# Performance work log

Hardware: AMD Instinct MI355X
Metric: run time of the kernel (lower is better)

## Reference

```python
import jax, jax.numpy as jnp
import numpy as np

G = 56          # voxel grid resolution per axis
N = 65536
K = 27          # 3x3x3 kernel offsets
C_IN = 128
C_OUT = 128


def _build_rulebook():
    """Submanifold conv rulebook: for each kernel offset, (input_row, output_row) pairs.

    Padded to P=N pairs per offset; invalid pairs use in_idx=0 and out_idx=N
    (a dummy output slot that is dropped), so shapes are static.
    """
    rng = np.random.default_rng(0)
    keys = np.sort(rng.choice(G ** 3, size=N, replace=False)).astype(np.int64)
    x = keys // (G * G)
    y = (keys // G) % G
    z = keys % G
    in_idx = np.zeros((K, N), dtype=np.int32)
    out_idx = np.full((K, N), N, dtype=np.int32)
    k = 0
    for dx in (-1, 0, 1):
        for dy in (-1, 0, 1):
            for dz in (-1, 0, 1):
                nx, ny, nz = x + dx, y + dy, z + dz
                valid = (nx >= 0) & (nx < G) & (ny >= 0) & (ny < G) & (nz >= 0) & (nz < G)
                nkey = (nx * G + ny) * G + nz
                pos = np.searchsorted(keys, np.clip(nkey, 0, G ** 3 - 1))
                pos = np.clip(pos, 0, N - 1)
                found = valid & (keys[pos] == nkey)
                cnt = int(found.sum())
                in_idx[k, :cnt] = pos[found]
                out_idx[k, :cnt] = np.nonzero(found)[0]
                k += 1
    return jnp.asarray(in_idx), jnp.asarray(out_idx)


def setup_inputs() -> dict:
    key = jax.random.key(0)
    k1, k2, k3 = jax.random.split(key, 3)
    fan_in = K * C_IN
    features = jax.random.normal(k1, (N, C_IN), dtype=jnp.float32)
    weight = jax.random.normal(k2, (K, C_IN, C_OUT), dtype=jnp.float32) * (1.0 / np.sqrt(fan_in))
    bias = jax.random.normal(k3, (C_OUT,), dtype=jnp.float32) * 0.01
    in_idx, out_idx = _build_rulebook()
    return {"features": features, "weight": weight, "bias": bias,
            "in_idx": in_idx, "out_idx": out_idx}


def reference(features, weight, bias, in_idx, out_idx):
    # gather: [K, P, C_in]
    gathered = features[in_idx]
    # per-offset GEMM: [K, P, C_out]
    contrib = jnp.einsum('kpc,kcd->kpd', gathered, weight)
    n = features.shape[0]
    c_out = weight.shape[-1]
    # scatter-accumulate into N real rows + 1 dummy row for padded pairs
    out = jnp.zeros((n + 1, c_out), dtype=features.dtype)
    out = out.at[out_idx.reshape(-1)].add(contrib.reshape(-1, c_out))
    return out[:n] + bias
```

## Files before the change

### kernel.cpp

```cpp
#include <hip/hip_runtime.h>
#include <hip/hip_bf16.h>
#include <stdint.h>

#define NV   65536
#define KOFF 27
#define CIN  128
#define COUT 128

typedef __bf16 bf16x8 __attribute__((ext_vector_type(8)));
typedef float  f32x4  __attribute__((ext_vector_type(4)));

__device__ __forceinline__ void async_copy16(void* lds, const void* g) {
    __builtin_amdgcn_global_load_lds(
        (const __attribute__((address_space(1))) void*)g,
        (__attribute__((address_space(3))) void*)lds,
        16, 0, 0);
}


__global__ void k_prep_feat(const float* __restrict__ f,
                            __hip_bfloat16* __restrict__ fb,
                            int total, int nvalid) {
    int i = blockIdx.x * 256 + threadIdx.x;
    if (i < total) {
        float v = (i < nvalid) ? f[i] : 0.0f;
        fb[i] = __float2bfloat16(v);
    }
}

__global__ void k_prep_w(const float* __restrict__ w,
                         __hip_bfloat16* __restrict__ wt) {
    int i = blockIdx.x * 256 + threadIdx.x;
    if (i < KOFF * CIN * COUT) {
        int k    = i >> 14;
        int cin  = (i >> 7) & 127;
        int cout = i & 127;
        wt[k * 16384 + cout * 128 + cin] = __float2bfloat16(w[i]);
    }
}

__global__ void k_init_nbr(int* __restrict__ nbr, int total) {
    int i = blockIdx.x * 256 + threadIdx.x;
    if (i < total) nbr[i] = NV;
}

__global__ void k_scatter_nbr(const int* __restrict__ in_idx,
                              const int* __restrict__ out_idx,
                              int* __restrict__ nbr) {
    int i = blockIdx.x * 256 + threadIdx.x;
    if (i < KOFF * NV) {
        int k = i >> 16;
        int o = out_idx[i];
        nbr[k * (NV + 1) + o] = in_idx[i];
    }
}

__global__ __launch_bounds__(256, 2)
void sp_conv_main(const __hip_bfloat16* __restrict__ feats,
                  const __hip_bfloat16* __restrict__ wt,
                  const int* __restrict__ nbr,
                  const float* __restrict__ bias,
                  float* __restrict__ out) {
    __shared__ unsigned char smem[65536];
    unsigned char* smA = smem;
    unsigned char* smB = smem + 32768;

    const int t   = threadIdx.x;
    const int bid = blockIdx.x;
    const int tile0 = ((bid & 7) * 64 + (bid >> 3)) * 128;

    const int w    = t >> 6;
    const int lane = t & 63;
    const int lr   = lane & 15;
    const int quad = lane >> 4;
    const int m0   = (w >> 1) * 64;
    const int n0   = (w & 1) * 64;

    const int srow   = t >> 4;
    const int sbyte  = ((t & 15) ^ srow) * 16;

    f32x4 acc[4][4] = {};

    const unsigned char* featsB = (const unsigned char*)feats;
    const unsigned char* wtB    = (const unsigned char*)wt;

    for (int k = 0; k < KOFF; ++k) {
        const int* nbrk = nbr + k * (NV + 1) + tile0;
        const unsigned char* wk = wtB + (size_t)k * 32768;
        #pragma unroll
        for (int i = 0; i < 8; ++i) {
            int r = i * 16 + srow;
            int arow = nbrk[r];
            async_copy16(smA + i * 4096 + t * 16,
                         featsB + (size_t)arow * 256 + sbyte);
            async_copy16(smB + i * 4096 + t * 16,
                         wk + r * 256 + sbyte);
        }
        __syncthreads();

        #pragma unroll
        for (int ks = 0; ks < 4; ++ks) {
            bf16x8 af[4], bfr[4];
            #pragma unroll
            for (int mt = 0; mt < 4; ++mt) {
                int row = m0 + mt * 16 + lr;
                int pch = ((ks * 4 + quad) ^ lr) * 16;
                af[mt] = *(const bf16x8*)(smA + row * 256 + pch);
            }
            #pragma unroll
            for (int nt = 0; nt < 4; ++nt) {
                int row = n0 + nt * 16 + lr;
                int pch = ((ks * 4 + quad) ^ lr) * 16;
                bfr[nt] = *(const bf16x8*)(smB + row * 256 + pch);
            }
            #pragma unroll
            for (int mt = 0; mt < 4; ++mt)
                #pragma unroll
                for (int nt = 0; nt < 4; ++nt)
                    acc[mt][nt] = __builtin_amdgcn_mfma_f32_16x16x32_bf16(
                        af[mt], bfr[nt], acc[mt][nt], 0, 0, 0);
        }
        __syncthreads();
    }

    float bv[4];
    #pragma unroll
    for (int nt = 0; nt < 4; ++nt) bv[nt] = bias[n0 + nt * 16 + lr];

    #pragma unroll
    for (int mt = 0; mt < 4; ++mt) {
        #pragma unroll
        for (int nt = 0; nt < 4; ++nt) {
            #pragma unroll
            for (int r = 0; r < 4; ++r) {
                int grow = tile0 + m0 + mt * 16 + quad * 4 + r;
                out[(size_t)grow * COUT + n0 + nt * 16 + lr] =
                    acc[mt][nt][r] + bv[nt];
            }
        }
    }
}


extern "C" void kernel_launch(void* const* d_in, const int* in_sizes, int n_in,
                              void* d_out, int out_size, void* d_ws, size_t ws_size,
                              hipStream_t stream) {
    const float* features = (const float*)d_in[0];
    const float* weight   = (const float*)d_in[1];
    const float* bias     = (const float*)d_in[2];
    const int*   in_idx   = (const int*)d_in[3];
    const int*   out_idx  = (const int*)d_in[4];
    float* out = (float*)d_out;

    uint8_t* ws = (uint8_t*)d_ws;
    size_t off = 0;
    __hip_bfloat16* feats_bf = (__hip_bfloat16*)(ws + off);
    off += (size_t)(NV + 1) * CIN * 2;
    off = (off + 255) & ~(size_t)255;
    __hip_bfloat16* wt_bf = (__hip_bfloat16*)(ws + off);
    off += (size_t)KOFF * CIN * COUT * 2;
    off = (off + 255) & ~(size_t)255;
    int* nbr = (int*)(ws + off);

    {
        int total = (NV + 1) * CIN;
        k_prep_feat<<<(total + 255) / 256, 256, 0, stream>>>(
            features, feats_bf, total, NV * CIN);
    }
    {
        int total = KOFF * CIN * COUT;
        k_prep_w<<<(total + 255) / 256, 256, 0, stream>>>(weight, wt_bf);
    }
    {
        int total = KOFF * (NV + 1);
        k_init_nbr<<<(total + 255) / 256, 256, 0, stream>>>(nbr, total);
    }
    {
        int total = KOFF * NV;
        k_scatter_nbr<<<(total + 255) / 256, 256, 0, stream>>>(
            in_idx, out_idx, nbr);
    }
    sp_conv_main<<<NV / 128, 256, 0, stream>>>(feats_bf, wt_bf, nbr, bias, out);
}
```

Baseline: 176.8 us.

## Vectorize prep kernels, memset neighbor table, prefetch next-offset neighbor indices

The feature conversion kernel now handles 8 elements per thread with float4 loads and 16-byte stores. The scatter kernel reads int4 index vectors. The neighbor-init kernel is replaced by a 0xFF memset, and the -1 sentinel is clamped to the zero dummy row with an unsigned min. In the main kernel, the neighbor indices for the next offset are loaded after the barrier so their global latency overlaps the MFMA work, at the cost of 8 extra live registers.

```diff
diff --git a/kernel.cpp b/kernel.cpp
--- a/kernel.cpp
+++ b/kernel.cpp
@@ -19,13 +19,27 @@
 
 
 __global__ void k_prep_feat(const float* __restrict__ f,
-                            __hip_bfloat16* __restrict__ fb,
-                            int total, int nvalid) {
+                            uint4* __restrict__ fb4,
+                            int total8, int nvalid8) {
     int i = blockIdx.x * 256 + threadIdx.x;
-    if (i < total) {
-        float v = (i < nvalid) ? f[i] : 0.0f;
-        fb[i] = __float2bfloat16(v);
-    }
+    if (i >= total8) return;
+    union { uint4 u; __hip_bfloat16 h[8]; } p;
+    if (i < nvalid8) {
+        const float4* f4 = (const float4*)f;
+        float4 a = f4[i * 2];
+        float4 b = f4[i * 2 + 1];
+        p.h[0] = __float2bfloat16(a.x);
+        p.h[1] = __float2bfloat16(a.y);
+        p.h[2] = __float2bfloat16(a.z);
+        p.h[3] = __float2bfloat16(a.w);
+        p.h[4] = __float2bfloat16(b.x);
+        p.h[5] = __float2bfloat16(b.y);
+        p.h[6] = __float2bfloat16(b.z);
+        p.h[7] = __float2bfloat16(b.w);
+    } else {
+        p.u = make_uint4(0, 0, 0, 0);
+    }
+    fb4[i] = p.u;
 }
 
 __global__ void k_prep_w(const float* __restrict__ w,
@@ -39,19 +53,19 @@
     }
 }
 
-__global__ void k_init_nbr(int* __restrict__ nbr, int total) {
-    int i = blockIdx.x * 256 + threadIdx.x;
-    if (i < total) nbr[i] = NV;
-}
-
-__global__ void k_scatter_nbr(const int* __restrict__ in_idx,
-                              const int* __restrict__ out_idx,
+__global__ void k_scatter_nbr(const int4* __restrict__ in4,
+                              const int4* __restrict__ out4,
                               int* __restrict__ nbr) {
     int i = blockIdx.x * 256 + threadIdx.x;
-    if (i < KOFF * NV) {
-        int k = i >> 16;
-        int o = out_idx[i];
-        nbr[k * (NV + 1) + o] = in_idx[i];
+    if (i < KOFF * NV / 4) {
+        int k = i >> 14;
+        int4 ii = in4[i];
+        int4 oo = out4[i];
+        int* nb = nbr + k * (NV + 1);
+        nb[oo.x] = ii.x;
+        nb[oo.y] = ii.y;
+        nb[oo.z] = ii.z;
+        nb[oo.w] = ii.w;
     }
 }
 
@@ -84,19 +98,30 @@
     const unsigned char* featsB = (const unsigned char*)feats;
     const unsigned char* wtB    = (const unsigned char*)wt;
 
+    int arows[8];
+    {
+        const int* nbr0 = nbr + tile0;
+        #pragma unroll
+        for (int i = 0; i < 8; ++i) arows[i] = nbr0[i * 16 + srow];
+    }
+
     for (int k = 0; k < KOFF; ++k) {
-        const int* nbrk = nbr + k * (NV + 1) + tile0;
         const unsigned char* wk = wtB + (size_t)k * 32768;
         #pragma unroll
         for (int i = 0; i < 8; ++i) {
-            int r = i * 16 + srow;
-            int arow = nbrk[r];
+            unsigned ar = min((unsigned)arows[i], (unsigned)NV);
             async_copy16(smA + i * 4096 + t * 16,
-                         featsB + (size_t)arow * 256 + sbyte);
+                         featsB + (size_t)ar * 256 + sbyte);
             async_copy16(smB + i * 4096 + t * 16,
-                         wk + r * 256 + sbyte);
+                         wk + (i * 16 + srow) * 256 + sbyte);
         }
         __syncthreads();
+
+        if (k + 1 < KOFF) {
+            const int* nbrn = nbr + (k + 1) * (NV + 1) + tile0;
+            #pragma unroll
+            for (int i = 0; i < 8; ++i) arows[i] = nbrn[i * 16 + srow];
+        }
 
         #pragma unroll
         for (int ks = 0; ks < 4; ++ks) {
@@ -163,22 +188,20 @@
     int* nbr = (int*)(ws + off);
 
     {
-        int total = (NV + 1) * CIN;
-        k_prep_feat<<<(total + 255) / 256, 256, 0, stream>>>(
-            features, feats_bf, total, NV * CIN);
+        int total8  = (NV + 1) * CIN / 8;
+        int nvalid8 = NV * CIN / 8;
+        k_prep_feat<<<(total8 + 255) / 256, 256, 0, stream>>>(
+            features, (uint4*)feats_bf, total8, nvalid8);
     }
     {
         int total = KOFF * CIN * COUT;
         k_prep_w<<<(total + 255) / 256, 256, 0, stream>>>(weight, wt_bf);
     }
-    {
-        int total = KOFF * (NV + 1);
-        k_init_nbr<<<(total + 255) / 256, 256, 0, stream>>>(nbr, total);
-    }
-    {
-        int total = KOFF * NV;
-        k_scatter_nbr<<<(total + 255) / 256, 256, 0, stream>>>(
-            in_idx, out_idx, nbr);
+    hipMemsetAsync(nbr, 0xFF, (size_t)KOFF * (NV + 1) * 4, stream);
+    {
+        int total4 = KOFF * NV / 4;
+        k_scatter_nbr<<<(total4 + 255) / 256, 256, 0, stream>>>(
+            (const int4*)in_idx, (const int4*)out_idx, nbr);
     }
     sp_conv_main<<<NV / 128, 256, 0, stream>>>(feats_bf, wt_bf, nbr, bias, out);
 }
```

Measured after the change: 169.0 us. -4.4%, faster.
